# Optimization experiments

Hardware: AMD Instinct MI355X
Metric: run time of the kernel (lower is better)

## Reference

```python
import jax, jax.numpy as jnp
import numpy as np
import math

HIDDEN = 4096
NUM_HEADS = 32
HEAD_DIM = HIDDEN // NUM_HEADS  # 128
SCALE = 1.0 / HEAD_DIM          # JAIS uses 1/d, not 1/sqrt(d)


def _alibi_slopes(n_heads: int) -> np.ndarray:
    cp2 = 2 ** math.floor(math.log2(n_heads))
    base = 2 ** (-2 ** (-(math.log2(cp2) - 3)))
    slopes = base ** np.arange(1, cp2 + 1, dtype=np.float32)
    if cp2 != n_heads:
        extra_base = 2 ** (-2 ** (-(math.log2(2 * cp2) - 3)))
        n_rem = min(cp2, n_heads - cp2)
        extra = extra_base ** np.arange(1, 1 + 2 * n_rem, 2, dtype=np.float32)
        slopes = np.concatenate([slopes, extra])
    return slopes.astype(np.float32)


def setup_inputs() -> dict:
    key = jax.random.key(0)
    k1, k2, k3, k4, k5 = jax.random.split(key, 5)
    B, S = 2, 2048
    return {
        "hidden_states": jax.random.normal(k1, (B, S, HIDDEN), dtype=jnp.float32),
        "w_attn": jax.random.normal(k2, (HIDDEN, 3 * HIDDEN), dtype=jnp.float32) * 0.02,
        "b_attn": jnp.zeros((3 * HIDDEN,), dtype=jnp.float32),
        "w_proj": jax.random.normal(k3, (HIDDEN, HIDDEN), dtype=jnp.float32) * 0.02,
        "b_proj": jnp.zeros((HIDDEN,), dtype=jnp.float32),
    }


def reference(hidden_states, w_attn, b_attn, w_proj, b_proj):
    B, S, _ = hidden_states.shape
    H, D = NUM_HEADS, HEAD_DIM

    # c_attn: fused QKV projection
    qkv = hidden_states @ w_attn + b_attn            # [B, S, 3*HIDDEN]
    q, k, v = jnp.split(qkv, 3, axis=-1)
    q = q.reshape(B, S, H, D)
    k = k.reshape(B, S, H, D)
    v = v.reshape(B, S, H, D)

    # attention scores with 1/d scaling
    scores = jnp.einsum("bqhd,bkhd->bhqk", q, k) * SCALE  # [B, H, S, S]

    # ALiBi bias: slope_h * (j - i), causal mask j <= i
    slopes = jnp.asarray(_alibi_slopes(H))                # [H]
    pos = jnp.arange(S)
    rel = pos[None, :] - pos[:, None]                     # j - i, [S, S]
    bias = slopes[:, None, None] * rel[None, :, :]        # [H, S, S]
    causal = rel <= 0
    scores = jnp.where(causal[None, None], scores + bias[None], -jnp.inf)

    attn = jax.nn.softmax(scores, axis=-1)
    out = jnp.einsum("bhqk,bkhd->bqhd", attn, v).reshape(B, S, HIDDEN)

    # c_proj
    return out @ w_proj + b_proj
```

## Files before the change

### kernel.cpp

```cpp
#include <hip/hip_runtime.h>
#include <hip/hip_bf16.h>
#include <cstdint>
#include <cstddef>

#define HIDDEN_ 4096
#define NHEAD 32
#define HDIM 128
#define SEQ 2048
#define BATCH 2
#define MROWS (BATCH * SEQ)
#define QKVN (3 * HIDDEN_)

typedef __bf16 bf16;
typedef __bf16 bf16x8 __attribute__((ext_vector_type(8)));
typedef float f32x4 __attribute__((ext_vector_type(4)));

#define AS1 __attribute__((address_space(1)))
#define AS3 __attribute__((address_space(3)))
#define PH_BAR do { asm volatile("" ::: "memory"); __builtin_amdgcn_s_barrier(); asm volatile("" ::: "memory"); } while (0)
#define MFMA_(d, a_, b_) (d) = __builtin_amdgcn_mfma_f32_16x16x32_bf16((a_), (b_), (d), 0, 0, 0)

__global__ __launch_bounds__(256) void cast_bf16_k(const float* __restrict__ in,
                                                   bf16* __restrict__ out, int n) {
  int i = (blockIdx.x * 256 + threadIdx.x) * 8;
  if (i >= n) return;
  f32x4 a = *(const f32x4*)(in + i);
  f32x4 b = *(const f32x4*)(in + i + 4);
  bf16x8 o;
  o[0] = (bf16)a[0]; o[1] = (bf16)a[1]; o[2] = (bf16)a[2]; o[3] = (bf16)a[3];
  o[4] = (bf16)b[0]; o[5] = (bf16)b[1]; o[6] = (bf16)b[2]; o[7] = (bf16)b[3];
  *(bf16x8*)(out + i) = o;
}

__global__ __launch_bounds__(256) void transpose_cast_k(const float* __restrict__ in,
                                                        bf16* __restrict__ out,
                                                        int R, int C) {
  __shared__ float tile[64][65];
  const int c0 = blockIdx.x * 64, r0 = blockIdx.y * 64;
  const int tr = threadIdx.x >> 4;
  const int tc4 = (threadIdx.x & 15) * 4;
#pragma unroll
  for (int p = 0; p < 4; p++) {
    const int r = p * 16 + tr;
    f32x4 v = *(const f32x4*)&in[(size_t)(r0 + r) * C + c0 + tc4];
    tile[r][tc4 + 0] = v[0]; tile[r][tc4 + 1] = v[1];
    tile[r][tc4 + 2] = v[2]; tile[r][tc4 + 3] = v[3];
  }
  __syncthreads();
  const int oc = threadIdx.x >> 3;
  const int or8 = (threadIdx.x & 7) * 8;
#pragma unroll
  for (int p = 0; p < 2; p++) {
    const int c = p * 32 + oc;
    bf16x8 o;
#pragma unroll
    for (int j = 0; j < 8; j++) o[j] = (bf16)tile[or8 + j][c];
    *(bf16x8*)&out[(size_t)(c0 + c) * R + r0 + or8] = o;
  }
}

template <int EPI>
__global__ __launch_bounds__(512, 2) void gemm256_k(
    const bf16* __restrict__ A, const bf16* __restrict__ BT,
    const float* __restrict__ bias, float* __restrict__ outF,
    bf16* __restrict__ Qb, bf16* __restrict__ Kb, bf16* __restrict__ Vt,
    int M, int N, int K, int nbx) {
  __shared__ char lds[131072];
  char* const A0 = lds;
  char* const A1 = lds + 32768;
  char* const B0 = lds + 65536;
  char* const B1 = lds + 98304;

  const int tid = threadIdx.x;
  const int w = tid >> 6, l = tid & 63;
  const int lg = l >> 4, cl = l & 15;
  const int wm = (w >> 2) * 128;
  const int wn = (w & 3) * 64;

  const int cpx = (int)gridDim.x >> 3;
  const int bid = blockIdx.x;
  const int swz = (bid & 7) * cpx + (bid >> 3);
  const int bx = swz % nbx, by = swz / nbx;
  const int m0 = by * 256, n0 = bx * 256;

  const int NT = K >> 6;
  const int NI = K >> 7;

  const bf16* gA[2][2]; const bf16* gB[2][2];
#pragma unroll
  for (int half = 0; half < 2; ++half)
#pragma unroll
    for (int i = 0; i < 2; ++i) {
      const int ci = i * 512 + tid;
      const int r = ci >> 3;
      const int cb = ((ci & 7) << 4) ^ ((r & 7) << 4);
      gA[half][i] = A + (size_t)(m0 + half * 128 + r) * K + (cb >> 1);
      gB[half][i] = BT + (size_t)(n0 + half * 128 + r) * K + (cb >> 1);
    }

  int offA[8][2], offB[4][2];
#pragma unroll
  for (int mf = 0; mf < 8; ++mf) {
    const int r = wm + mf * 16 + cl;
#pragma unroll
    for (int ks = 0; ks < 2; ++ks)
      offA[mf][ks] = r * 128 + ((ks * 64 + lg * 16) ^ ((r & 7) << 4));
  }
#pragma unroll
  for (int nf = 0; nf < 4; ++nf) {
    const int r = wn + nf * 16 + cl;
#pragma unroll
    for (int ks = 0; ks < 2; ++ks)
      offB[nf][ks] = r * 128 + ((ks * 64 + lg * 16) ^ ((r & 7) << 4));
  }

  auto stageA = [&](char* buf, int half, int kt) {
#pragma unroll
    for (int i = 0; i < 2; ++i) {
      const int ci = i * 512 + tid;
      __builtin_amdgcn_global_load_lds((const AS1 void*)(gA[half][i] + kt * 64),
                                       (AS3 void*)(buf + half * 16384 + ci * 16), 16, 0, 0);
    }
  };
  auto stageB = [&](char* buf, int half, int kt) {
#pragma unroll
    for (int i = 0; i < 2; ++i) {
      const int ci = i * 512 + tid;
      __builtin_amdgcn_global_load_lds((const AS1 void*)(gB[half][i] + kt * 64),
                                       (AS3 void*)(buf + half * 16384 + ci * 16), 16, 0, 0);
    }
  };
  auto rdA = [&](const char* buf, int mf, int ks) -> bf16x8 {
    return *(const bf16x8*)(buf + offA[mf][ks]);
  };
  auto rdB = [&](const char* buf, int nf, int ks) -> bf16x8 {
    return *(const bf16x8*)(buf + offB[nf][ks]);
  };

  f32x4 acc[8][4] = {};
  bf16x8 alo[4][2], ahi[4][2], blo[2][2], bhi[2][2];

  stageA(A0, 0, 0); stageB(B0, 0, 0); stageA(A0, 1, 0); stageB(B0, 1, 0);
  stageB(B1, 0, 1); stageB(B1, 1, 1);
  asm volatile("s_waitcnt vmcnt(4)" ::: "memory");
  PH_BAR;

  for (int j = 0; j < NI; ++j) {
    const int tw = 2 * j + 1;
    const int tu = (2 * j + 2) & (NT - 1);
    const int tv = (2 * j + 3) & (NT - 1);

#pragma unroll
    for (int mf = 0; mf < 4; ++mf) { alo[mf][0] = rdA(A0, mf, 0); alo[mf][1] = rdA(A0, mf, 1); }
#pragma unroll
    for (int nf = 0; nf < 2; ++nf) { blo[nf][0] = rdB(B0, nf, 0); blo[nf][1] = rdB(B0, nf, 1); }
#pragma unroll
    for (int nf = 0; nf < 2; ++nf) { bhi[nf][0] = rdB(B0, 2 + nf, 0); bhi[nf][1] = rdB(B0, 2 + nf, 1); }
    stageA(A1, 0, tw);
    stageA(A1, 1, tw);
    __builtin_amdgcn_s_setprio(1);
#pragma unroll
    for (int mf = 0; mf < 4; ++mf)
#pragma unroll
      for (int nf = 0; nf < 2; ++nf)
#pragma unroll
        for (int ks = 0; ks < 2; ++ks) MFMA_(acc[mf][nf], alo[mf][ks], blo[nf][ks]);
#pragma unroll
    for (int mf = 0; mf < 4; ++mf)
#pragma unroll
      for (int nf = 0; nf < 2; ++nf)
#pragma unroll
        for (int ks = 0; ks < 2; ++ks) MFMA_(acc[mf][2 + nf], alo[mf][ks], bhi[nf][ks]);
    __builtin_amdgcn_s_setprio(0);
    PH_BAR;

#pragma unroll
    for (int mf = 0; mf < 4; ++mf) { ahi[mf][0] = rdA(A0, 4 + mf, 0); ahi[mf][1] = rdA(A0, 4 + mf, 1); }
    stageB(B0, 0, tu);
    stageB(B0, 1, tu);
    __builtin_amdgcn_s_setprio(1);
#pragma unroll
    for (int mf = 0; mf < 4; ++mf)
#pragma unroll
      for (int nf = 0; nf < 2; ++nf)
#pragma unroll
        for (int ks = 0; ks < 2; ++ks) MFMA_(acc[4 + mf][2 + nf], ahi[mf][ks], bhi[nf][ks]);
#pragma unroll
    for (int mf = 0; mf < 4; ++mf)
#pragma unroll
      for (int nf = 0; nf < 2; ++nf)
#pragma unroll
        for (int ks = 0; ks < 2; ++ks) MFMA_(acc[4 + mf][nf], ahi[mf][ks], blo[nf][ks]);
    __builtin_amdgcn_s_setprio(0);
    asm volatile("s_waitcnt vmcnt(4)" ::: "memory");
    PH_BAR;

#pragma unroll
    for (int mf = 0; mf < 4; ++mf) { alo[mf][0] = rdA(A1, mf, 0); alo[mf][1] = rdA(A1, mf, 1); }
#pragma unroll
    for (int nf = 0; nf < 2; ++nf) { blo[nf][0] = rdB(B1, nf, 0); blo[nf][1] = rdB(B1, nf, 1); }
#pragma unroll
    for (int nf = 0; nf < 2; ++nf) { bhi[nf][0] = rdB(B1, 2 + nf, 0); bhi[nf][1] = rdB(B1, 2 + nf, 1); }
    stageA(A0, 0, tu);
    stageA(A0, 1, tu);
    __builtin_amdgcn_s_setprio(1);
#pragma unroll
    for (int mf = 0; mf < 4; ++mf)
#pragma unroll
      for (int nf = 0; nf < 2; ++nf)
#pragma unroll
        for (int ks = 0; ks < 2; ++ks) MFMA_(acc[mf][nf], alo[mf][ks], blo[nf][ks]);
#pragma unroll
    for (int mf = 0; mf < 4; ++mf)
#pragma unroll
      for (int nf = 0; nf < 2; ++nf)
#pragma unroll
        for (int ks = 0; ks < 2; ++ks) MFMA_(acc[mf][2 + nf], alo[mf][ks], bhi[nf][ks]);
    __builtin_amdgcn_s_setprio(0);
    PH_BAR;

#pragma unroll
    for (int mf = 0; mf < 4; ++mf) { ahi[mf][0] = rdA(A1, 4 + mf, 0); ahi[mf][1] = rdA(A1, 4 + mf, 1); }
    stageB(B1, 0, tv);
    stageB(B1, 1, tv);
    __builtin_amdgcn_s_setprio(1);
#pragma unroll
    for (int mf = 0; mf < 4; ++mf)
#pragma unroll
      for (int nf = 0; nf < 2; ++nf)
#pragma unroll
        for (int ks = 0; ks < 2; ++ks) MFMA_(acc[4 + mf][2 + nf], ahi[mf][ks], bhi[nf][ks]);
#pragma unroll
    for (int mf = 0; mf < 4; ++mf)
#pragma unroll
      for (int nf = 0; nf < 2; ++nf)
#pragma unroll
        for (int ks = 0; ks < 2; ++ks) MFMA_(acc[4 + mf][nf], ahi[mf][ks], blo[nf][ks]);
    __builtin_amdgcn_s_setprio(0);
    asm volatile("s_waitcnt vmcnt(4)" ::: "memory");
    PH_BAR;
  }

#pragma unroll
  for (int mf = 0; mf < 8; ++mf) {
#pragma unroll
    for (int nf = 0; nf < 4; ++nf) {
      const int col = n0 + wn + nf * 16 + cl;
      const float bv = bias[col];
#pragma unroll
      for (int r = 0; r < 4; ++r) {
        const int row = m0 + wm + mf * 16 + lg * 4 + r;
        const float v = acc[mf][nf][r] + bv;
        if (EPI == 0) {
          const int which = col >> 12, rem = col & 4095;
          const int h = rem >> 7, d = rem & 127;
          const int b = row >> 11, s = row & 2047;
          const size_t bh = (size_t)b * NHEAD + h;
          if (which == 0)      Qb[(bh * SEQ + s) * HDIM + d] = (bf16)v;
          else if (which == 1) Kb[(bh * SEQ + s) * HDIM + d] = (bf16)v;
          else                 Vt[(bh * HDIM + d) * SEQ + s] = (bf16)v;
        } else {
          outF[(size_t)row * N + col] = v;
        }
      }
    }
  }
}

__global__ __launch_bounds__(256, 2) void attn_k(const bf16* __restrict__ Qb,
                                                 const bf16* __restrict__ Kb,
                                                 const bf16* __restrict__ Vt,
                                                 bf16* __restrict__ ctx) {
  __shared__ bf16 Ks[2][64 * 128];
  __shared__ bf16 Vs[2][128 * 64];
  __shared__ bf16 Pl[4][32 * 64];
  const int tid = threadIdx.x, w = tid >> 6, l = tid & 63;
  const int bid = blockIdx.x;
  const int qt = 15 - (bid >> 6);
  const int bh = bid & 63;
  const int h = bh & (NHEAD - 1), b = bh >> 5;
  const int qbase = qt * 128 + w * 32;
  const int nt = 2 * qt + 2;
  const float slope = exp2f(-0.25f * (float)(h + 1));
  const float scale = 1.0f / 128.0f;
  const int lg = l >> 4, cl = l & 15;

  const bf16* Qp = Qb + (size_t)bh * SEQ * HDIM;
  const bf16* Kp = Kb + (size_t)bh * SEQ * HDIM;
  const bf16* Vp = Vt + (size_t)bh * HDIM * SEQ;
  char* plb = (char*)&Pl[w][0];

  bf16x8 qf[2][4];
#pragma unroll
  for (int mfr = 0; mfr < 2; ++mfr)
#pragma unroll
    for (int kb = 0; kb < 4; ++kb)
      qf[mfr][kb] = *(const bf16x8*)&Qp[(size_t)(qbase + mfr * 16 + cl) * HDIM + kb * 32 + lg * 8];

  float mi[2][4], li[2][4];
#pragma unroll
  for (int mfr = 0; mfr < 2; ++mfr)
#pragma unroll
    for (int r = 0; r < 4; ++r) { mi[mfr][r] = -3.0e38f; li[mfr][r] = 0.0f; }
  f32x4 oacc[2][8] = {};

  auto stage = [&](int buf, int t) {
    const int kv0 = t * 64;
#pragma unroll
    for (int i = 0; i < 4; i++) {
      const int ci = i * 256 + tid;
      {
        const int r = ci >> 4;
        const int cbl = ((ci & 15) << 4) ^ ((r & 7) << 4);
        const bf16* src = Kp + (size_t)(kv0 + r) * HDIM + (cbl >> 1);
        __builtin_amdgcn_global_load_lds(
            (const AS1 void*)src,
            (AS3 void*)((char*)&Ks[buf][0] + ci * 16), 16, 0, 0);
      }
      {
        const int r = ci >> 3;
        const int cbl = ((ci & 7) << 4) ^ ((r & 7) << 4);
        const bf16* src = Vp + (size_t)r * SEQ + kv0 + (cbl >> 1);
        __builtin_amdgcn_global_load_lds(
            (const AS1 void*)src,
            (AS3 void*)((char*)&Vs[buf][0] + ci * 16), 16, 0, 0);
      }
    }
  };

  stage(0, 0);
  __syncthreads();

  for (int t = 0; t < nt; ++t) {
    const int cur = t & 1;
    if (t + 1 < nt) stage(cur ^ 1, t + 1);
    const int kv0 = t * 64;

    if (kv0 <= qbase + 31) {
      char* ksb = (char*)&Ks[cur][0];
      char* vsb = (char*)&Vs[cur][0];
      f32x4 sacc[2][4] = {};
      __builtin_amdgcn_s_setprio(1);
#pragma unroll
      for (int nb = 0; nb < 4; nb++) {
#pragma unroll
        for (int kb = 0; kb < 4; kb++) {
          const int row = nb * 16 + cl;
          const int cb = (kb * 64 + lg * 16) ^ ((row & 7) << 4);
          bf16x8 kf = *(const bf16x8*)(ksb + row * 256 + cb);
#pragma unroll
          for (int mfr = 0; mfr < 2; ++mfr)
            sacc[mfr][nb] = __builtin_amdgcn_mfma_f32_16x16x32_bf16(qf[mfr][kb], kf, sacc[mfr][nb], 0, 0, 0);
        }
      }
      __builtin_amdgcn_s_setprio(0);
#pragma unroll
      for (int mfr = 0; mfr < 2; ++mfr) {
        float pm[4];
#pragma unroll
        for (int r = 0; r < 4; r++) pm[r] = -3.0e38f;
#pragma unroll
        for (int nb = 0; nb < 4; nb++) {
          const int kv = kv0 + nb * 16 + cl;
#pragma unroll
          for (int r = 0; r < 4; r++) {
            const int q = qbase + mfr * 16 + lg * 4 + r;
            float v = sacc[mfr][nb][r] * scale + slope * (float)(kv - q);
            v = (kv <= q) ? v : -3.0e38f;
            sacc[mfr][nb][r] = v;
            pm[r] = fmaxf(pm[r], v);
          }
        }
#pragma unroll
        for (int r = 0; r < 4; r++) {
          pm[r] = fmaxf(pm[r], __shfl_xor(pm[r], 1));
          pm[r] = fmaxf(pm[r], __shfl_xor(pm[r], 2));
          pm[r] = fmaxf(pm[r], __shfl_xor(pm[r], 4));
          pm[r] = fmaxf(pm[r], __shfl_xor(pm[r], 8));
        }
        int need = 0;
#pragma unroll
        for (int r = 0; r < 4; r++) need |= (pm[r] > mi[mfr][r] + 8.0f) ? 1 : 0;
        const bool resc = __any(need);
        float alpha[4];
        if (resc) {
#pragma unroll
          for (int r = 0; r < 4; r++) {
            const float nm = fmaxf(mi[mfr][r], pm[r]);
            alpha[r] = __expf(mi[mfr][r] - nm);
            mi[mfr][r] = nm;
          }
        }
        float rs[4] = {0.0f, 0.0f, 0.0f, 0.0f};
#pragma unroll
        for (int nb = 0; nb < 4; nb++) {
#pragma unroll
          for (int r = 0; r < 4; r++) {
            const float p = __expf(sacc[mfr][nb][r] - mi[mfr][r]);
            rs[r] += p;
            const int row = mfr * 16 + lg * 4 + r;
            *(bf16*)(plb + row * 128 + ((((nb * 16 + cl) << 1)) ^ ((row & 7) << 4))) = (bf16)p;
          }
        }
#pragma unroll
        for (int r = 0; r < 4; r++) {
          rs[r] += __shfl_xor(rs[r], 1);
          rs[r] += __shfl_xor(rs[r], 2);
          rs[r] += __shfl_xor(rs[r], 4);
          rs[r] += __shfl_xor(rs[r], 8);
        }
        if (resc) {
#pragma unroll
          for (int r = 0; r < 4; r++) li[mfr][r] = li[mfr][r] * alpha[r] + rs[r];
#pragma unroll
          for (int db = 0; db < 8; db++)
#pragma unroll
            for (int r = 0; r < 4; r++) oacc[mfr][db][r] *= alpha[r];
        } else {
#pragma unroll
          for (int r = 0; r < 4; r++) li[mfr][r] += rs[r];
        }
      }
      bf16x8 pa[2][2];
#pragma unroll
      for (int mfr = 0; mfr < 2; ++mfr)
#pragma unroll
        for (int ks = 0; ks < 2; ks++) {
          const int cb = (ks * 64 + lg * 16) ^ ((cl & 7) << 4);
          pa[mfr][ks] = *(const bf16x8*)(plb + (mfr * 16 + cl) * 128 + cb);
        }
      __builtin_amdgcn_s_setprio(1);
#pragma unroll
      for (int db = 0; db < 8; db++) {
#pragma unroll
        for (int ks = 0; ks < 2; ks++) {
          const int row = db * 16 + cl;
          const int cb = (ks * 64 + lg * 16) ^ ((row & 7) << 4);
          bf16x8 vf = *(const bf16x8*)(vsb + row * 128 + cb);
#pragma unroll
          for (int mfr = 0; mfr < 2; ++mfr)
            oacc[mfr][db] = __builtin_amdgcn_mfma_f32_16x16x32_bf16(pa[mfr][ks], vf, oacc[mfr][db], 0, 0, 0);
        }
      }
      __builtin_amdgcn_s_setprio(0);
    }
    __syncthreads();
  }

#pragma unroll
  for (int mfr = 0; mfr < 2; ++mfr) {
    float inv[4];
#pragma unroll
    for (int r = 0; r < 4; r++) inv[r] = 1.0f / li[mfr][r];
#pragma unroll
    for (int db = 0; db < 8; db++) {
#pragma unroll
      for (int r = 0; r < 4; r++) {
        const int q = qbase + mfr * 16 + lg * 4 + r;
        ctx[((size_t)(b * SEQ + q)) * HIDDEN_ + h * HDIM + db * 16 + cl] = (bf16)(oacc[mfr][db][r] * inv[r]);
      }
    }
  }
}

extern "C" void kernel_launch(void* const* d_in, const int* in_sizes, int n_in,
                              void* d_out, int out_size, void* d_ws, size_t ws_size,
                              hipStream_t stream) {
  const float* hs     = (const float*)d_in[0];
  const float* w_attn = (const float*)d_in[1];
  const float* b_attn = (const float*)d_in[2];
  const float* w_proj = (const float*)d_in[3];
  const float* b_proj = (const float*)d_in[4];
  float* out = (float*)d_out;

  char* ws = (char*)d_ws;
  bf16* Xb  = (bf16*)(ws + 0);
  bf16* WaT = (bf16*)(ws + 33554432);
  bf16* WpT = (bf16*)(ws + 134217728);
  bf16* Qb  = (bf16*)(ws + 167772160);
  bf16* Kb  = (bf16*)(ws + 201326592);
  bf16* Vt  = (bf16*)(ws + 234881024);
  bf16* ctx = (bf16*)(ws + 268435456);

  cast_bf16_k<<<(MROWS * HIDDEN_) / (256 * 8), 256, 0, stream>>>(hs, Xb, MROWS * HIDDEN_);
  transpose_cast_k<<<dim3(QKVN / 64, HIDDEN_ / 64), 256, 0, stream>>>(w_attn, WaT, HIDDEN_, QKVN);
  transpose_cast_k<<<dim3(HIDDEN_ / 64, HIDDEN_ / 64), 256, 0, stream>>>(w_proj, WpT, HIDDEN_, HIDDEN_);

  gemm256_k<0><<<dim3((QKVN / 256) * (MROWS / 256)), 512, 0, stream>>>(
      Xb, WaT, b_attn, nullptr, Qb, Kb, Vt, MROWS, QKVN, HIDDEN_, QKVN / 256);

  attn_k<<<16 * 64, 256, 0, stream>>>(Qb, Kb, Vt, ctx);

  gemm256_k<1><<<dim3((HIDDEN_ / 256) * (MROWS / 256)), 512, 0, stream>>>(
      ctx, WpT, b_proj, out, nullptr, nullptr, nullptr, MROWS, HIDDEN_, HIDDEN_, HIDDEN_ / 256);
}
```

Before: 765.4 us.

## Shrink GEMM tile to 128x256 with K=32 triple-buffered pipeline

Replaces the 256x256 GEMM tile and its hand-unrolled double-buffered K=64 loop with a 128x256 tile, K step 32, and a three-stage rotating LDS buffer. LDS use drops to 72KB and launch bounds rise to 4 blocks per CU, aiming for more occupancy and twice as many blocks to even out load across CUs. In exchange each block reuses loaded data less, each K step does fewer MFMAs per barrier so barriers become relatively more frequent, and the interleaving of LDS reads with MFMAs is simpler.

```diff
diff --git a/kernel.cpp b/kernel.cpp
--- a/kernel.cpp
+++ b/kernel.cpp
@@ -60,189 +60,106 @@
 }
 
 template <int EPI>
-__global__ __launch_bounds__(512, 2) void gemm256_k(
+__global__ __launch_bounds__(512, 4) void gemm256_k(
     const bf16* __restrict__ A, const bf16* __restrict__ BT,
     const float* __restrict__ bias, float* __restrict__ outF,
     bf16* __restrict__ Qb, bf16* __restrict__ Kb, bf16* __restrict__ Vt,
     int M, int N, int K, int nbx) {
-  __shared__ char lds[131072];
-  char* const A0 = lds;
-  char* const A1 = lds + 32768;
-  char* const B0 = lds + 65536;
-  char* const B1 = lds + 98304;
+  __shared__ char lds[73728];
 
   const int tid = threadIdx.x;
   const int w = tid >> 6, l = tid & 63;
   const int lg = l >> 4, cl = l & 15;
-  const int wm = (w >> 2) * 128;
+  const int wm = (w >> 2) * 64;
   const int wn = (w & 3) * 64;
 
   const int cpx = (int)gridDim.x >> 3;
   const int bid = blockIdx.x;
   const int swz = (bid & 7) * cpx + (bid >> 3);
   const int bx = swz % nbx, by = swz / nbx;
-  const int m0 = by * 256, n0 = bx * 256;
-
-  const int NT = K >> 6;
-  const int NI = K >> 7;
-
-  const bf16* gA[2][2]; const bf16* gB[2][2];
-#pragma unroll
-  for (int half = 0; half < 2; ++half)
-#pragma unroll
-    for (int i = 0; i < 2; ++i) {
-      const int ci = i * 512 + tid;
-      const int r = ci >> 3;
-      const int cb = ((ci & 7) << 4) ^ ((r & 7) << 4);
-      gA[half][i] = A + (size_t)(m0 + half * 128 + r) * K + (cb >> 1);
-      gB[half][i] = BT + (size_t)(n0 + half * 128 + r) * K + (cb >> 1);
-    }
-
-  int offA[8][2], offB[4][2];
-#pragma unroll
-  for (int mf = 0; mf < 8; ++mf) {
+  const int m0 = by * 128, n0 = bx * 256;
+
+  const int NT = K >> 5;
+
+  const bf16* gA;
+  {
+    const int r = tid >> 2;
+    const int cb = ((tid & 3) << 4) ^ (((r >> 1) & 3) << 4);
+    gA = A + (size_t)(m0 + r) * K + (cb >> 1);
+  }
+  const bf16* gB[2];
+#pragma unroll
+  for (int i = 0; i < 2; ++i) {
+    const int ci = i * 512 + tid;
+    const int r = ci >> 2;
+    const int cb = ((ci & 3) << 4) ^ (((r >> 1) & 3) << 4);
+    gB[i] = BT + (size_t)(n0 + r) * K + (cb >> 1);
+  }
+
+  int offA[4], offB[4];
+#pragma unroll
+  for (int mf = 0; mf < 4; ++mf) {
     const int r = wm + mf * 16 + cl;
-#pragma unroll
-    for (int ks = 0; ks < 2; ++ks)
-      offA[mf][ks] = r * 128 + ((ks * 64 + lg * 16) ^ ((r & 7) << 4));
+    offA[mf] = r * 64 + ((lg * 16) ^ (((r >> 1) & 3) << 4));
   }
 #pragma unroll
   for (int nf = 0; nf < 4; ++nf) {
     const int r = wn + nf * 16 + cl;
-#pragma unroll
-    for (int ks = 0; ks < 2; ++ks)
-      offB[nf][ks] = r * 128 + ((ks * 64 + lg * 16) ^ ((r & 7) << 4));
-  }
-
-  auto stageA = [&](char* buf, int half, int kt) {
+    offB[nf] = r * 64 + ((lg * 16) ^ (((r >> 1) & 3) << 4));
+  }
+
+  auto stageA = [&](char* buf, int kt) {
+    __builtin_amdgcn_global_load_lds((const AS1 void*)(gA + kt * 32),
+                                     (AS3 void*)(buf + tid * 16), 16, 0, 0);
+  };
+  auto stageB = [&](char* buf, int kt) {
 #pragma unroll
     for (int i = 0; i < 2; ++i) {
-      const int ci = i * 512 + tid;
-      __builtin_amdgcn_global_load_lds((const AS1 void*)(gA[half][i] + kt * 64),
-                                       (AS3 void*)(buf + half * 16384 + ci * 16), 16, 0, 0);
+      __builtin_amdgcn_global_load_lds((const AS1 void*)(gB[i] + kt * 32),
+                                       (AS3 void*)(buf + (i * 512 + tid) * 16), 16, 0, 0);
     }
   };
-  auto stageB = [&](char* buf, int half, int kt) {
-#pragma unroll
-    for (int i = 0; i < 2; ++i) {
-      const int ci = i * 512 + tid;
-      __builtin_amdgcn_global_load_lds((const AS1 void*)(gB[half][i] + kt * 64),
-                                       (AS3 void*)(buf + half * 16384 + ci * 16), 16, 0, 0);
-    }
-  };
-  auto rdA = [&](const char* buf, int mf, int ks) -> bf16x8 {
-    return *(const bf16x8*)(buf + offA[mf][ks]);
-  };
-  auto rdB = [&](const char* buf, int nf, int ks) -> bf16x8 {
-    return *(const bf16x8*)(buf + offB[nf][ks]);
-  };
-
-  f32x4 acc[8][4] = {};
-  bf16x8 alo[4][2], ahi[4][2], blo[2][2], bhi[2][2];
-
-  stageA(A0, 0, 0); stageB(B0, 0, 0); stageA(A0, 1, 0); stageB(B0, 1, 0);
-  stageB(B1, 0, 1); stageB(B1, 1, 1);
-  asm volatile("s_waitcnt vmcnt(4)" ::: "memory");
+
+  f32x4 acc[4][4] = {};
+
+  char* Ar0 = lds;             char* Br0 = lds + 24576;
+  char* Ar1 = lds + 8192;      char* Br1 = lds + 40960;
+  char* Ar2 = lds + 16384;     char* Br2 = lds + 57344;
+
+  stageA(Ar0, 0); stageB(Br0, 0);
+  stageA(Ar1, 1); stageB(Br1, 1);
+  asm volatile("s_waitcnt vmcnt(3)" ::: "memory");
   PH_BAR;
 
-  for (int j = 0; j < NI; ++j) {
-    const int tw = 2 * j + 1;
-    const int tu = (2 * j + 2) & (NT - 1);
-    const int tv = (2 * j + 3) & (NT - 1);
-
-#pragma unroll
-    for (int mf = 0; mf < 4; ++mf) { alo[mf][0] = rdA(A0, mf, 0); alo[mf][1] = rdA(A0, mf, 1); }
-#pragma unroll
-    for (int nf = 0; nf < 2; ++nf) { blo[nf][0] = rdB(B0, nf, 0); blo[nf][1] = rdB(B0, nf, 1); }
-#pragma unroll
-    for (int nf = 0; nf < 2; ++nf) { bhi[nf][0] = rdB(B0, 2 + nf, 0); bhi[nf][1] = rdB(B0, 2 + nf, 1); }
-    stageA(A1, 0, tw);
-    stageA(A1, 1, tw);
+  for (int t = 0; t < NT; ++t) {
+    if (t + 2 < NT) { stageA(Ar2, t + 2); stageB(Br2, t + 2); }
+
+    bf16x8 af[4], bfr[4];
+#pragma unroll
+    for (int nf = 0; nf < 4; ++nf) bfr[nf] = *(const bf16x8*)(Br0 + offB[nf]);
+#pragma unroll
+    for (int mf = 0; mf < 4; ++mf) af[mf] = *(const bf16x8*)(Ar0 + offA[mf]);
+
     __builtin_amdgcn_s_setprio(1);
 #pragma unroll
     for (int mf = 0; mf < 4; ++mf)
 #pragma unroll
-      for (int nf = 0; nf < 2; ++nf)
-#pragma unroll
-        for (int ks = 0; ks < 2; ++ks) MFMA_(acc[mf][nf], alo[mf][ks], blo[nf][ks]);
-#pragma unroll
-    for (int mf = 0; mf < 4; ++mf)
-#pragma unroll
-      for (int nf = 0; nf < 2; ++nf)
-#pragma unroll
-        for (int ks = 0; ks < 2; ++ks) MFMA_(acc[mf][2 + nf], alo[mf][ks], bhi[nf][ks]);
+      for (int nf = 0; nf < 4; ++nf) MFMA_(acc[mf][nf], af[mf], bfr[nf]);
     __builtin_amdgcn_s_setprio(0);
+
+    if (t + 2 < NT) {
+      asm volatile("s_waitcnt vmcnt(3)" ::: "memory");
+    } else {
+      asm volatile("s_waitcnt vmcnt(0)" ::: "memory");
+    }
     PH_BAR;
 
-#pragma unroll
-    for (int mf = 0; mf < 4; ++mf) { ahi[mf][0] = rdA(A0, 4 + mf, 0); ahi[mf][1] = rdA(A0, 4 + mf, 1); }
-    stageB(B0, 0, tu);
-    stageB(B0, 1, tu);
-    __builtin_amdgcn_s_setprio(1);
-#pragma unroll
-    for (int mf = 0; mf < 4; ++mf)
-#pragma unroll
-      for (int nf = 0; nf < 2; ++nf)
-#pragma unroll
-        for (int ks = 0; ks < 2; ++ks) MFMA_(acc[4 + mf][2 + nf], ahi[mf][ks], bhi[nf][ks]);
-#pragma unroll
-    for (int mf = 0; mf < 4; ++mf)
-#pragma unroll
-      for (int nf = 0; nf < 2; ++nf)
-#pragma unroll
-        for (int ks = 0; ks < 2; ++ks) MFMA_(acc[4 + mf][nf], ahi[mf][ks], blo[nf][ks]);
-    __builtin_amdgcn_s_setprio(0);
-    asm volatile("s_waitcnt vmcnt(4)" ::: "memory");
-    PH_BAR;
-
-#pragma unroll
-    for (int mf = 0; mf < 4; ++mf) { alo[mf][0] = rdA(A1, mf, 0); alo[mf][1] = rdA(A1, mf, 1); }
-#pragma unroll
-    for (int nf = 0; nf < 2; ++nf) { blo[nf][0] = rdB(B1, nf, 0); blo[nf][1] = rdB(B1, nf, 1); }
-#pragma unroll
-    for (int nf = 0; nf < 2; ++nf) { bhi[nf][0] = rdB(B1, 2 + nf, 0); bhi[nf][1] = rdB(B1, 2 + nf, 1); }
-    stageA(A0, 0, tu);
-    stageA(A0, 1, tu);
-    __builtin_amdgcn_s_setprio(1);
-#pragma unroll
-    for (int mf = 0; mf < 4; ++mf)
-#pragma unroll
-      for (int nf = 0; nf < 2; ++nf)
-#pragma unroll
-        for (int ks = 0; ks < 2; ++ks) MFMA_(acc[mf][nf], alo[mf][ks], blo[nf][ks]);
-#pragma unroll
-    for (int mf = 0; mf < 4; ++mf)
-#pragma unroll
-      for (int nf = 0; nf < 2; ++nf)
-#pragma unroll
-        for (int ks = 0; ks < 2; ++ks) MFMA_(acc[mf][2 + nf], alo[mf][ks], bhi[nf][ks]);
-    __builtin_amdgcn_s_setprio(0);
-    PH_BAR;
-
-#pragma unroll
-    for (int mf = 0; mf < 4; ++mf) { ahi[mf][0] = rdA(A1, 4 + mf, 0); ahi[mf][1] = rdA(A1, 4 + mf, 1); }
-    stageB(B1, 0, tv);
-    stageB(B1, 1, tv);
-    __builtin_amdgcn_s_setprio(1);
-#pragma unroll
-    for (int mf = 0; mf < 4; ++mf)
-#pragma unroll
-      for (int nf = 0; nf < 2; ++nf)
-#pragma unroll
-        for (int ks = 0; ks < 2; ++ks) MFMA_(acc[4 + mf][2 + nf], ahi[mf][ks], bhi[nf][ks]);
-#pragma unroll
-    for (int mf = 0; mf < 4; ++mf)
-#pragma unroll
-      for (int nf = 0; nf < 2; ++nf)
-#pragma unroll
-        for (int ks = 0; ks < 2; ++ks) MFMA_(acc[4 + mf][nf], ahi[mf][ks], blo[nf][ks]);
-    __builtin_amdgcn_s_setprio(0);
-    asm volatile("s_waitcnt vmcnt(4)" ::: "memory");
-    PH_BAR;
-  }
-
-#pragma unroll
-  for (int mf = 0; mf < 8; ++mf) {
+    char* ta = Ar0; Ar0 = Ar1; Ar1 = Ar2; Ar2 = ta;
+    char* tb = Br0; Br0 = Br1; Br1 = Br2; Br2 = tb;
+  }
+
+#pragma unroll
+  for (int mf = 0; mf < 4; ++mf) {
 #pragma unroll
     for (int nf = 0; nf < 4; ++nf) {
       const int col = n0 + wn + nf * 16 + cl;
@@ -486,11 +403,11 @@
   transpose_cast_k<<<dim3(QKVN / 64, HIDDEN_ / 64), 256, 0, stream>>>(w_attn, WaT, HIDDEN_, QKVN);
   transpose_cast_k<<<dim3(HIDDEN_ / 64, HIDDEN_ / 64), 256, 0, stream>>>(w_proj, WpT, HIDDEN_, HIDDEN_);
 
-  gemm256_k<0><<<dim3((QKVN / 256) * (MROWS / 256)), 512, 0, stream>>>(
+  gemm256_k<0><<<dim3((QKVN / 256) * (MROWS / 128)), 512, 0, stream>>>(
       Xb, WaT, b_attn, nullptr, Qb, Kb, Vt, MROWS, QKVN, HIDDEN_, QKVN / 256);
 
   attn_k<<<16 * 64, 256, 0, stream>>>(Qb, Kb, Vt, ctx);
 
-  gemm256_k<1><<<dim3((HIDDEN_ / 256) * (MROWS / 256)), 512, 0, stream>>>(
+  gemm256_k<1><<<dim3((HIDDEN_ / 256) * (MROWS / 128)), 512, 0, stream>>>(
       ctx, WpT, b_proj, out, nullptr, nullptr, nullptr, MROWS, HIDDEN_, HIDDEN_, HIDDEN_ / 256);
 }
```

Result: slower. 961.4 us (+25.6%).

## Split GEMM main loop into finer barrier-synchronized phases with deeper A prefetch

Applied to the files above, without the earlier changes.

Restructures the GEMM main loop from 4 into 8 phases per iteration. Each phase issues a smaller group of LDS reads or async global-to-LDS stages, then waits at a barrier and an lgkmcnt(0) fence before running a smaller batch of MFMAs. The A-tile prefetch is split in halves and one half is issued earlier, which raises the vmcnt wait threshold from 4 to 6. The intent is to interleave memory traffic with MFMA work across waves, in the style of ping-pong scheduling. It doubles the number of barriers and adds explicit wait fences, which could stall the waves.

```diff
diff --git a/kernel.cpp b/kernel.cpp
--- a/kernel.cpp
+++ b/kernel.cpp
@@ -18,6 +18,7 @@
 #define AS1 __attribute__((address_space(1)))
 #define AS3 __attribute__((address_space(3)))
 #define PH_BAR do { asm volatile("" ::: "memory"); __builtin_amdgcn_s_barrier(); asm volatile("" ::: "memory"); } while (0)
+#define LGKM0_FENCE do { asm volatile("s_waitcnt lgkmcnt(0)" ::: "memory"); __builtin_amdgcn_sched_barrier(0); } while (0)
 #define MFMA_(d, a_, b_) (d) = __builtin_amdgcn_mfma_f32_16x16x32_bf16((a_), (b_), (d), 0, 0, 0)
 
 __global__ __launch_bounds__(256) void cast_bf16_k(const float* __restrict__ in,
@@ -141,8 +142,8 @@
   bf16x8 alo[4][2], ahi[4][2], blo[2][2], bhi[2][2];
 
   stageA(A0, 0, 0); stageB(B0, 0, 0); stageA(A0, 1, 0); stageB(B0, 1, 0);
-  stageB(B1, 0, 1); stageB(B1, 1, 1);
-  asm volatile("s_waitcnt vmcnt(4)" ::: "memory");
+  stageB(B1, 0, 1); stageB(B1, 1, 1); stageA(A1, 0, 1);
+  asm volatile("s_waitcnt vmcnt(6)" ::: "memory");
   PH_BAR;
 
   for (int j = 0; j < NI; ++j) {
@@ -154,17 +155,24 @@
     for (int mf = 0; mf < 4; ++mf) { alo[mf][0] = rdA(A0, mf, 0); alo[mf][1] = rdA(A0, mf, 1); }
 #pragma unroll
     for (int nf = 0; nf < 2; ++nf) { blo[nf][0] = rdB(B0, nf, 0); blo[nf][1] = rdB(B0, nf, 1); }
+    stageA(A1, 1, tw);
+    PH_BAR;
+    LGKM0_FENCE;
+    __builtin_amdgcn_s_setprio(1);
+#pragma unroll
+    for (int mf = 0; mf < 4; ++mf)
+#pragma unroll
+      for (int nf = 0; nf < 2; ++nf)
+#pragma unroll
+        for (int ks = 0; ks < 2; ++ks) MFMA_(acc[mf][nf], alo[mf][ks], blo[nf][ks]);
+    __builtin_amdgcn_s_setprio(0);
+    PH_BAR;
+
 #pragma unroll
     for (int nf = 0; nf < 2; ++nf) { bhi[nf][0] = rdB(B0, 2 + nf, 0); bhi[nf][1] = rdB(B0, 2 + nf, 1); }
-    stageA(A1, 0, tw);
-    stageA(A1, 1, tw);
-    __builtin_amdgcn_s_setprio(1);
-#pragma unroll
-    for (int mf = 0; mf < 4; ++mf)
-#pragma unroll
-      for (int nf = 0; nf < 2; ++nf)
-#pragma unroll
-        for (int ks = 0; ks < 2; ++ks) MFMA_(acc[mf][nf], alo[mf][ks], blo[nf][ks]);
+    PH_BAR;
+    LGKM0_FENCE;
+    __builtin_amdgcn_s_setprio(1);
 #pragma unroll
     for (int mf = 0; mf < 4; ++mf)
 #pragma unroll
@@ -178,6 +186,8 @@
     for (int mf = 0; mf < 4; ++mf) { ahi[mf][0] = rdA(A0, 4 + mf, 0); ahi[mf][1] = rdA(A0, 4 + mf, 1); }
     stageB(B0, 0, tu);
     stageB(B0, 1, tu);
+    PH_BAR;
+    LGKM0_FENCE;
     __builtin_amdgcn_s_setprio(1);
 #pragma unroll
     for (int mf = 0; mf < 4; ++mf)
@@ -185,6 +195,12 @@
       for (int nf = 0; nf < 2; ++nf)
 #pragma unroll
         for (int ks = 0; ks < 2; ++ks) MFMA_(acc[4 + mf][2 + nf], ahi[mf][ks], bhi[nf][ks]);
+    __builtin_amdgcn_s_setprio(0);
+    PH_BAR;
+
+    stageA(A0, 0, tu);
+    PH_BAR;
+    __builtin_amdgcn_s_setprio(1);
 #pragma unroll
     for (int mf = 0; mf < 4; ++mf)
 #pragma unroll
@@ -192,24 +208,31 @@
 #pragma unroll
         for (int ks = 0; ks < 2; ++ks) MFMA_(acc[4 + mf][nf], ahi[mf][ks], blo[nf][ks]);
     __builtin_amdgcn_s_setprio(0);
-    asm volatile("s_waitcnt vmcnt(4)" ::: "memory");
+    asm volatile("s_waitcnt vmcnt(6)" ::: "memory");
     PH_BAR;
 
 #pragma unroll
     for (int mf = 0; mf < 4; ++mf) { alo[mf][0] = rdA(A1, mf, 0); alo[mf][1] = rdA(A1, mf, 1); }
 #pragma unroll
     for (int nf = 0; nf < 2; ++nf) { blo[nf][0] = rdB(B1, nf, 0); blo[nf][1] = rdB(B1, nf, 1); }
+    stageA(A0, 1, tu);
+    PH_BAR;
+    LGKM0_FENCE;
+    __builtin_amdgcn_s_setprio(1);
+#pragma unroll
+    for (int mf = 0; mf < 4; ++mf)
+#pragma unroll
+      for (int nf = 0; nf < 2; ++nf)
+#pragma unroll
+        for (int ks = 0; ks < 2; ++ks) MFMA_(acc[mf][nf], alo[mf][ks], blo[nf][ks]);
+    __builtin_amdgcn_s_setprio(0);
+    PH_BAR;
+
 #pragma unroll
     for (int nf = 0; nf < 2; ++nf) { bhi[nf][0] = rdB(B1, 2 + nf, 0); bhi[nf][1] = rdB(B1, 2 + nf, 1); }
-    stageA(A0, 0, tu);
-    stageA(A0, 1, tu);
-    __builtin_amdgcn_s_setprio(1);
-#pragma unroll
-    for (int mf = 0; mf < 4; ++mf)
-#pragma unroll
-      for (int nf = 0; nf < 2; ++nf)
-#pragma unroll
-        for (int ks = 0; ks < 2; ++ks) MFMA_(acc[mf][nf], alo[mf][ks], blo[nf][ks]);
+    PH_BAR;
+    LGKM0_FENCE;
+    __builtin_amdgcn_s_setprio(1);
 #pragma unroll
     for (int mf = 0; mf < 4; ++mf)
 #pragma unroll
@@ -223,6 +246,8 @@
     for (int mf = 0; mf < 4; ++mf) { ahi[mf][0] = rdA(A1, 4 + mf, 0); ahi[mf][1] = rdA(A1, 4 + mf, 1); }
     stageB(B1, 0, tv);
     stageB(B1, 1, tv);
+    PH_BAR;
+    LGKM0_FENCE;
     __builtin_amdgcn_s_setprio(1);
 #pragma unroll
     for (int mf = 0; mf < 4; ++mf)
@@ -230,6 +255,12 @@
       for (int nf = 0; nf < 2; ++nf)
 #pragma unroll
         for (int ks = 0; ks < 2; ++ks) MFMA_(acc[4 + mf][2 + nf], ahi[mf][ks], bhi[nf][ks]);
+    __builtin_amdgcn_s_setprio(0);
+    PH_BAR;
+
+    stageA(A1, 0, tv);
+    PH_BAR;
+    __builtin_amdgcn_s_setprio(1);
 #pragma unroll
     for (int mf = 0; mf < 4; ++mf)
 #pragma unroll
@@ -237,7 +268,7 @@
 #pragma unroll
         for (int ks = 0; ks < 2; ++ks) MFMA_(acc[4 + mf][nf], ahi[mf][ks], blo[nf][ks]);
     __builtin_amdgcn_s_setprio(0);
-    asm volatile("s_waitcnt vmcnt(4)" ::: "memory");
+    asm volatile("s_waitcnt vmcnt(6)" ::: "memory");
     PH_BAR;
   }
 
```

New measurement: 768.2 us. About the same (+0.4%).
